# Kernel optimization log

Hardware: AMD Instinct MI355X
Metric: run time of the kernel (lower is better)

## Reference

```python
import jax, jax.numpy as jnp
import numpy as np

D_MODEL = 1024
N_HEADS = 16
D_HEAD = D_MODEL // N_HEADS
B, S = 2, 2048


def setup_inputs() -> dict:
    key = jax.random.key(0)
    ks = jax.random.split(key, 8)
    scale = 1.0 / np.sqrt(D_MODEL)
    return {
        "x": jax.random.normal(ks[0], (B, S, D_MODEL), dtype=jnp.float32),
        "Wq": jax.random.normal(ks[1], (D_MODEL, D_MODEL), dtype=jnp.float32) * scale,
        "bq": jnp.zeros((D_MODEL,), dtype=jnp.float32),
        "Wk": jax.random.normal(ks[2], (D_MODEL, D_MODEL), dtype=jnp.float32) * scale,
        "bk": jnp.zeros((D_MODEL,), dtype=jnp.float32),
        "Wv": jax.random.normal(ks[3], (D_MODEL, D_MODEL), dtype=jnp.float32) * scale,
        "bv": jnp.zeros((D_MODEL,), dtype=jnp.float32),
        "Wo": jax.random.normal(ks[4], (D_MODEL, D_MODEL), dtype=jnp.float32) * scale,
    }


def reference(x, Wq, bq, Wk, bk, Wv, bv, Wo):
    Bsz, Slen, D = x.shape
    # projections -> [B, H, S, Dh]
    def split_heads(t):
        return t.reshape(Bsz, Slen, N_HEADS, D_HEAD).transpose(0, 2, 1, 3)
    q = split_heads(x @ Wq + bq)
    k = split_heads(x @ Wk + bk)
    v = split_heads(x @ Wv + bv)
    scale = jnp.sqrt(jnp.float32(D_HEAD))
    scores = jnp.einsum('bhsd,bhtd->bhst', q, k) / scale  # [B,H,S,S]
    causal_mask = jnp.tril(jnp.ones((Slen, Slen), dtype=jnp.bool_))
    scores = jnp.where(causal_mask, scores, jnp.finfo(scores.dtype).min)
    attn = jax.nn.softmax(scores, axis=-1)
    # deterministic=True path: dropout is identity
    out = jnp.einsum('bhst,bhtd->bhsd', attn, v)
    out = out.transpose(0, 2, 1, 3).reshape(Bsz, Slen, D)
    return out @ Wo
```

## Files before the change

### kernel.cpp

```cpp
#include <hip/hip_runtime.h>
#include <hip/hip_bf16.h>

#define BATCH   2
#define SEQ     2048
#define DMODEL  1024
#define NHEADS  16
#define DHEAD   64
#define MROWS   (BATCH*SEQ)
#define NBH     (BATCH*NHEADS)

typedef float  f32x4  __attribute__((ext_vector_type(4)));
typedef short  s16x4  __attribute__((ext_vector_type(4)));
typedef short  s16x8  __attribute__((ext_vector_type(8)));
typedef __bf16 bf16x8 __attribute__((ext_vector_type(8)));

__device__ __forceinline__ short f2bf(float f) {
  union { float f; unsigned u; } v; v.f = f;
  return (short)((v.u + 0x7fffu + ((v.u >> 16) & 1u)) >> 16);
}
__device__ __forceinline__ float bf2f(short s) {
  union { unsigned u; float f; } v; v.u = ((unsigned)(unsigned short)s) << 16;
  return v.f;
}

__global__ void convert_x(const float* __restrict__ x, short* __restrict__ xb) {
  int i = (blockIdx.x * 256 + threadIdx.x) * 4;
  float4 v = *(const float4*)(x + i);
  s16x4 o = { f2bf(v.x), f2bf(v.y), f2bf(v.z), f2bf(v.w) };
  *(s16x4*)(xb + i) = o;
}

__global__ void transpose_w(const float* __restrict__ Wq, const float* __restrict__ Wk,
                            const float* __restrict__ Wv, const float* __restrict__ Wo,
                            short* __restrict__ WtQKV, short* __restrict__ WtO) {
  __shared__ float t[32][33];
  const float* W; short* Wt;
  int z = blockIdx.z;
  if      (z == 0) { W = Wq; Wt = WtQKV; }
  else if (z == 1) { W = Wk; Wt = WtQKV + (1u << 20); }
  else if (z == 2) { W = Wv; Wt = WtQKV + (2u << 20); }
  else             { W = Wo; Wt = WtO; }
  int n0 = blockIdx.x * 32, k0 = blockIdx.y * 32;
  int tx = threadIdx.x, ty = threadIdx.y;
  #pragma unroll
  for (int i = 0; i < 32; i += 8) t[ty + i][tx] = W[(k0 + ty + i) * DMODEL + n0 + tx];
  __syncthreads();
  #pragma unroll
  for (int i = 0; i < 32; i += 8) Wt[(n0 + ty + i) * DMODEL + k0 + tx] = f2bf(t[tx][ty + i]);
}

template<int MT, int NT, int EPI>
__global__ __launch_bounds__(256) void gemm_bf16(
    const short* __restrict__ A, const short* __restrict__ Bt,
    const float* __restrict__ bq, const float* __restrict__ bk, const float* __restrict__ bv,
    short* __restrict__ qb, short* __restrict__ kb, short* __restrict__ vt,
    float* __restrict__ out)
{
  constexpr int K = DMODEL, BK = 32;
  constexpr int WM = MT / 2, WN = NT / 2;
  constexpr int TM = WM / 16, TN = WN / 16;
  constexpr int CA = MT * BK / 512;
  constexpr int CB = NT * BK / 512;
  constexpr int TP = 136;
  constexpr int SME = (EPI == 0) ? 128 * TP : (MT * BK + NT * BK);
  __shared__ short smem[SME];
  short* la = smem;
  short* lb = smem + MT * BK;
  const int tid = threadIdx.x;
  const int wave = tid >> 6, lane = tid & 63;
  const int quad = lane >> 4, l16 = lane & 15;
  const int wr = wave >> 1, wc = wave & 1;
  const int m0 = blockIdx.y * MT, n0 = blockIdx.x * NT;
  const int arow = lane >> 2, acol = (lane & 3) * 8;

  f32x4 acc[TM][TN] = {};

  for (int k0 = 0; k0 < K; k0 += BK) {
    for (int c = wave; c < CA; c += 4) {
      const short* gp = A + (m0 + c * 16 + arow) * K + k0 + acol;
      __builtin_amdgcn_global_load_lds((__attribute__((address_space(1))) void*)gp,
                                       (__attribute__((address_space(3))) void*)(la + c * 512),
                                       16, 0, 0);
    }
    for (int c = wave; c < CB; c += 4) {
      const short* gp = Bt + (n0 + c * 16 + arow) * K + k0 + acol;
      __builtin_amdgcn_global_load_lds((__attribute__((address_space(1))) void*)gp,
                                       (__attribute__((address_space(3))) void*)(lb + c * 512),
                                       16, 0, 0);
    }
    __syncthreads();
    bf16x8 af[TM], bfr[TN];
    #pragma unroll
    for (int i = 0; i < TM; ++i)
      af[i] = *(const bf16x8*)&la[(wr * WM + i * 16 + l16) * BK + quad * 8];
    #pragma unroll
    for (int j = 0; j < TN; ++j)
      bfr[j] = *(const bf16x8*)&lb[(wc * WN + j * 16 + l16) * BK + quad * 8];
    #pragma unroll
    for (int i = 0; i < TM; ++i)
      #pragma unroll
      for (int j = 0; j < TN; ++j)
        acc[i][j] = __builtin_amdgcn_mfma_f32_16x16x32_bf16(af[i], bfr[j], acc[i][j], 0, 0, 0);
    __syncthreads();
  }

  if constexpr (EPI == 0) {
    const bool isV = (n0 >= 2 * DMODEL);
    const float* bias; int nbase; float scl;
    if (n0 < DMODEL)          { bias = bq; nbase = 0;          scl = 0.125f * 1.44269504089f; }
    else if (n0 < 2 * DMODEL) { bias = bk; nbase = DMODEL;     scl = 1.f; }
    else                      { bias = bv; nbase = 2 * DMODEL; scl = 1.f; }
    #pragma unroll
    for (int j = 0; j < TN; ++j) {
      int coll = wc * WN + j * 16 + l16;
      float bias_v = bias[n0 - nbase + coll];
      #pragma unroll
      for (int i = 0; i < TM; ++i) {
        int rowl = wr * WM + i * 16 + quad * 4;
        #pragma unroll
        for (int r = 0; r < 4; ++r) {
          short v = f2bf((acc[i][j][r] + bias_v) * scl);
          if (isV) smem[coll * TP + rowl + r] = v;
          else     smem[(rowl + r) * TP + coll] = v;
        }
      }
    }
    __syncthreads();
    const int b = m0 >> 11, s0 = m0 & (SEQ - 1);
    const int rseg = tid & 15, rrow = tid >> 4;
    if (!isV) {
      short* dst = (n0 < DMODEL) ? qb : kb;
      #pragma unroll
      for (int it = 0; it < 8; ++it) {
        int row = it * 16 + rrow;
        int colg = (n0 - nbase) + rseg * 8;
        int h = colg >> 6, d = colg & 63;
        s16x8 v = *(const s16x8*)&smem[row * TP + rseg * 8];
        *(s16x8*)(dst + ((b * NHEADS + h) * SEQ + s0 + row) * DHEAD + d) = v;
      }
    } else {
      #pragma unroll
      for (int it = 0; it < 8; ++it) {
        int drow = it * 16 + rrow;
        int colg = (n0 - nbase) + drow;
        int h = colg >> 6, d = colg & 63;
        s16x8 v = *(const s16x8*)&smem[drow * TP + rseg * 8];
        *(s16x8*)(vt + ((b * NHEADS + h) * DHEAD + d) * SEQ + s0 + rseg * 8) = v;
      }
    }
  } else {
    #pragma unroll
    for (int i = 0; i < TM; ++i)
      #pragma unroll
      for (int r = 0; r < 4; ++r) {
        int mrow = m0 + wr * WM + i * 16 + quad * 4 + r;
        #pragma unroll
        for (int j = 0; j < TN; ++j)
          out[mrow * DMODEL + n0 + wc * WN + j * 16 + l16] = acc[i][j][r];
      }
    (void)bq; (void)bk; (void)bv; (void)qb; (void)kb; (void)vt;
  }
}


__global__ __launch_bounds__(256, 2) void attn_k(
    const short* __restrict__ qbp, const short* __restrict__ kbp,
    const short* __restrict__ vtb, short* __restrict__ oP, float* __restrict__ lP)
{
  __shared__ short kls[2][4096];
  __shared__ short vls[2][4096];
  const int tid = threadIdx.x, wave = tid >> 6, lane = tid & 63;
  const int quad = lane >> 4, l16 = lane & 15;
  const int half = blockIdx.x & 1;
  const int bh = (blockIdx.x >> 1) & 31;
  const int qg = blockIdx.x >> 6;
  const int qt = qg * 4 + wave;
  const int ma = qt * 16;
  const int mb = (127 - qt) * 16;
  const int nch = (127 - qg * 4) / 4 + 1;
  const short* Q  = qbp + bh * SEQ * DHEAD;
  const short* Kp = kbp + bh * SEQ * DHEAD;
  const short* Vt = vtb + bh * DHEAD * SEQ;

  bf16x8 qa0 = *(const bf16x8*)&Q[(ma + l16) * DHEAD + quad * 8];
  bf16x8 qa1 = *(const bf16x8*)&Q[(ma + l16) * DHEAD + 32 + quad * 8];
  bf16x8 qb0 = *(const bf16x8*)&Q[(mb + l16) * DHEAD + quad * 8];
  bf16x8 qb1 = *(const bf16x8*)&Q[(mb + l16) * DHEAD + 32 + quad * 8];

  float lA = 0.f, lB = 0.f;
  f32x4 oA[4] = {}, oB[4] = {};

  const int vdl = lane >> 3, vsl = lane & 7;

  auto stage = [&](int buf, int t0) {
    #pragma unroll
    for (int j = 0; j < 2; ++j) {
      int g = j * 4 + wave;
      const short* gp = Kp + (t0 + lane) * DHEAD + g * 8;
      __builtin_amdgcn_global_load_lds((__attribute__((address_space(1))) void*)gp,
                                       (__attribute__((address_space(3))) void*)&kls[buf][g * 512],
                                       16, 0, 0);
    }
    #pragma unroll
    for (int j = 0; j < 2; ++j) {
      int gd = j * 4 + wave;
      const short* gp = Vt + (gd * 8 + vdl) * SEQ + t0 + ((vsl ^ vdl) * 8);
      __builtin_amdgcn_global_load_lds((__attribute__((address_space(1))) void*)gp,
                                       (__attribute__((address_space(3))) void*)&vls[buf][gd * 512],
                                       16, 0, 0);
    }
  };

  auto frag = [&](const bf16x8 kf[4][2], const s16x4 vf[4][4], int t0, int mF,
                  bf16x8 f0, bf16x8 f1, float& lF, f32x4 oF[4]) {
    const int nlive = (mF - t0) / 16 + 1;
    #pragma unroll
    for (int t = 0; t < 4; ++t) {
      if (t < nlive) {
        f32x4 a = {};
        a = __builtin_amdgcn_mfma_f32_16x16x32_bf16(kf[t][0], f0, a, 0, 0, 0);
        a = __builtin_amdgcn_mfma_f32_16x16x32_bf16(kf[t][1], f1, a, 0, 0, 0);
        if (t0 + t * 16 == mF) {
          #pragma unroll
          for (int r = 0; r < 4; ++r)
            if (quad * 4 + r > l16) a[r] = -1e30f;
        }
        f32x4 p;
        #pragma unroll
        for (int r = 0; r < 4; ++r) p[r] = __builtin_amdgcn_exp2f(a[r]);
        lF += (p[0] + p[1]) + (p[2] + p[3]);
        __hip_bfloat162 c01 = __float22bfloat162_rn(float2{p[0], p[1]});
        __hip_bfloat162 c23 = __float22bfloat162_rn(float2{p[2], p[3]});
        union { unsigned u[2]; s16x4 s; } pu;
        pu.u[0] = *(unsigned*)&c01; pu.u[1] = *(unsigned*)&c23;
        #pragma unroll
        for (int dt = 0; dt < 4; ++dt)
          oF[dt] = __builtin_amdgcn_mfma_f32_16x16x16bf16_1k(pu.s, vf[t][dt], oF[dt], 0, 0, 0);
      }
    }
  };

  stage(0, half * 64);
  for (int c = half; c < nch; c += 2) {
    __syncthreads();
    if (c + 2 < nch) stage(((c >> 1) + 1) & 1, (c + 2) * 64);
    const int t0 = c * 64;
    const int buf = (c >> 1) & 1;
    bf16x8 kf[4][2];
    #pragma unroll
    for (int t = 0; t < 4; ++t)
      #pragma unroll
      for (int h = 0; h < 2; ++h)
        kf[t][h] = *(const bf16x8*)&kls[buf][((h * 4 + quad) * 64 + t * 16 + l16) * 8];
    s16x4 vf[4][4];
    #pragma unroll
    for (int t = 0; t < 4; ++t) {
      int gsw = ((t * 2 + (quad >> 1)) ^ (l16 & 7));
      #pragma unroll
      for (int dt = 0; dt < 4; ++dt)
        vf[t][dt] = *(const s16x4*)&vls[buf][((dt * 16 + l16) * 8 + gsw) * 8 + (quad & 1) * 4];
    }
    if (t0 <= mb) frag(kf, vf, t0, mb, qb0, qb1, lB, oB);
    if (t0 <= ma) frag(kf, vf, t0, ma, qa0, qa1, lA, oA);
  }

  lA += __shfl_xor(lA, 16, 64); lA += __shfl_xor(lA, 32, 64);
  lB += __shfl_xor(lB, 16, 64); lB += __shfl_xor(lB, 32, 64);
  float* lD = lP + (half * NBH + bh) * SEQ;
  if (quad == 0) { lD[ma + l16] = lA; lD[mb + l16] = lB; }
  short* oD = oP + ((half * NBH + bh) * SEQ) * DHEAD;
  #pragma unroll
  for (int r = 0; r < 4; ++r) {
    int sA = ma + quad * 4 + r, sB = mb + quad * 4 + r;
    #pragma unroll
    for (int dt = 0; dt < 4; ++dt) {
      oD[sA * DHEAD + dt * 16 + l16] = f2bf(oA[dt][r]);
      oD[sB * DHEAD + dt * 16 + l16] = f2bf(oB[dt][r]);
    }
  }
}

__global__ void attn_merge(const short* __restrict__ oP, const float* __restrict__ lP,
                           short* __restrict__ ob) {
  int idx = blockIdx.x * 256 + threadIdx.x;
  int d8 = idx & 7, s = (idx >> 3) & (SEQ - 1), bh = idx >> 14;
  s16x8 e = *(const s16x8*)&oP[((0   + bh) * SEQ + s) * DHEAD + d8 * 8];
  s16x8 o = *(const s16x8*)&oP[((NBH + bh) * SEQ + s) * DHEAD + d8 * 8];
  float linv = 1.0f / (lP[bh * SEQ + s] + lP[(NBH + bh) * SEQ + s]);
  s16x8 r;
  #pragma unroll
  for (int k = 0; k < 8; ++k) r[k] = f2bf((bf2f(e[k]) + bf2f(o[k])) * linv);
  int b = bh >> 4, h = bh & 15;
  *(s16x8*)&ob[(b * SEQ + s) * DMODEL + h * DHEAD + d8 * 8] = r;
}

extern "C" void kernel_launch(void* const* d_in, const int* in_sizes, int n_in,
                              void* d_out, int out_size, void* d_ws, size_t ws_size,
                              hipStream_t stream) {
  const float* x  = (const float*)d_in[0];
  const float* Wq = (const float*)d_in[1];
  const float* bq = (const float*)d_in[2];
  const float* Wk = (const float*)d_in[3];
  const float* bk = (const float*)d_in[4];
  const float* Wv = (const float*)d_in[5];
  const float* bv = (const float*)d_in[6];
  const float* Wo = (const float*)d_in[7];
  float* out = (float*)d_out;

  char* ws = (char*)d_ws;
  short* xb  = (short*)(ws);
  short* wtq = (short*)(ws + (8u  << 20));
  short* oP  = (short*)(ws);
  short* qb  = (short*)(ws + (16u << 20));
  short* kb  = (short*)(ws + (24u << 20));
  short* vt  = (short*)(ws + (32u << 20));
  short* ob  = (short*)(ws + (40u << 20));
  short* wto = (short*)(ws + (48u << 20));
  float* lP  = (float*)(ws + (50u << 20));

  convert_x<<<MROWS * DMODEL / 1024, 256, 0, stream>>>(x, xb);
  transpose_w<<<dim3(32, 32, 4), dim3(32, 8), 0, stream>>>(Wq, Wk, Wv, Wo, wtq, wto);

  gemm_bf16<128, 128, 0><<<dim3(3 * DMODEL / 128, MROWS / 128), 256, 0, stream>>>(
      xb, wtq, bq, bk, bv, qb, kb, vt, nullptr);

  attn_k<<<NBH * 16 * 2, 256, 0, stream>>>(qb, kb, vt, oP, lP);
  attn_merge<<<NBH * SEQ * 8 / 256, 256, 0, stream>>>(oP, lP, ob);

  gemm_bf16<64, 128, 1><<<dim3(DMODEL / 128, MROWS / 64), 256, 0, stream>>>(
      ob, wto, nullptr, nullptr, nullptr, nullptr, nullptr, nullptr, out);
}
```

Baseline: 198.6 us.

## Process four query tiles per wave in attention to reuse K/V fragments

Each wave of the attention kernel now handles four 16-row query tiles: two adjacent tiles from the front and their mirrored pair from the back, instead of one front/back pair. K and V fragments read from LDS are shared across all four tiles, and the grid is halved. This cuts LDS reads and global K/V staging per unit of work. The cost is more accumulator registers (16 f32x4 plus 8 Q fragments) and half as many blocks, which may reduce occupancy and parallelism on the device.

```diff
diff --git a/kernel.cpp b/kernel.cpp
--- a/kernel.cpp
+++ b/kernel.cpp
@@ -174,21 +174,22 @@
   const int half = blockIdx.x & 1;
   const int bh = (blockIdx.x >> 1) & 31;
   const int qg = blockIdx.x >> 6;
-  const int qt = qg * 4 + wave;
-  const int ma = qt * 16;
-  const int mb = (127 - qt) * 16;
-  const int nch = (127 - qg * 4) / 4 + 1;
+  const int qt1 = qg * 8 + wave * 2;
+  const int mF[4] = { qt1 * 16, (qt1 + 1) * 16, (126 - qt1) * 16, (127 - qt1) * 16 };
+  const int nch = (127 - 8 * qg) / 4 + 1;
   const short* Q  = qbp + bh * SEQ * DHEAD;
   const short* Kp = kbp + bh * SEQ * DHEAD;
   const short* Vt = vtb + bh * DHEAD * SEQ;
 
-  bf16x8 qa0 = *(const bf16x8*)&Q[(ma + l16) * DHEAD + quad * 8];
-  bf16x8 qa1 = *(const bf16x8*)&Q[(ma + l16) * DHEAD + 32 + quad * 8];
-  bf16x8 qb0 = *(const bf16x8*)&Q[(mb + l16) * DHEAD + quad * 8];
-  bf16x8 qb1 = *(const bf16x8*)&Q[(mb + l16) * DHEAD + 32 + quad * 8];
-
-  float lA = 0.f, lB = 0.f;
-  f32x4 oA[4] = {}, oB[4] = {};
+  bf16x8 qf[4][2];
+  #pragma unroll
+  for (int f = 0; f < 4; ++f) {
+    qf[f][0] = *(const bf16x8*)&Q[(mF[f] + l16) * DHEAD + quad * 8];
+    qf[f][1] = *(const bf16x8*)&Q[(mF[f] + l16) * DHEAD + 32 + quad * 8];
+  }
+
+  float lF[4] = {};
+  f32x4 oF[4][4] = {};
 
   const int vdl = lane >> 3, vsl = lane & 7;
 
@@ -211,71 +212,66 @@
     }
   };
 
-  auto frag = [&](const bf16x8 kf[4][2], const s16x4 vf[4][4], int t0, int mF,
-                  bf16x8 f0, bf16x8 f1, float& lF, f32x4 oF[4]) {
-    const int nlive = (mF - t0) / 16 + 1;
-    #pragma unroll
-    for (int t = 0; t < 4; ++t) {
-      if (t < nlive) {
-        f32x4 a = {};
-        a = __builtin_amdgcn_mfma_f32_16x16x32_bf16(kf[t][0], f0, a, 0, 0, 0);
-        a = __builtin_amdgcn_mfma_f32_16x16x32_bf16(kf[t][1], f1, a, 0, 0, 0);
-        if (t0 + t * 16 == mF) {
-          #pragma unroll
-          for (int r = 0; r < 4; ++r)
-            if (quad * 4 + r > l16) a[r] = -1e30f;
-        }
-        f32x4 p;
-        #pragma unroll
-        for (int r = 0; r < 4; ++r) p[r] = __builtin_amdgcn_exp2f(a[r]);
-        lF += (p[0] + p[1]) + (p[2] + p[3]);
-        __hip_bfloat162 c01 = __float22bfloat162_rn(float2{p[0], p[1]});
-        __hip_bfloat162 c23 = __float22bfloat162_rn(float2{p[2], p[3]});
-        union { unsigned u[2]; s16x4 s; } pu;
-        pu.u[0] = *(unsigned*)&c01; pu.u[1] = *(unsigned*)&c23;
-        #pragma unroll
-        for (int dt = 0; dt < 4; ++dt)
-          oF[dt] = __builtin_amdgcn_mfma_f32_16x16x16bf16_1k(pu.s, vf[t][dt], oF[dt], 0, 0, 0);
-      }
-    }
-  };
-
   stage(0, half * 64);
   for (int c = half; c < nch; c += 2) {
     __syncthreads();
     if (c + 2 < nch) stage(((c >> 1) + 1) & 1, (c + 2) * 64);
     const int t0 = c * 64;
     const int buf = (c >> 1) & 1;
-    bf16x8 kf[4][2];
-    #pragma unroll
-    for (int t = 0; t < 4; ++t)
-      #pragma unroll
-      for (int h = 0; h < 2; ++h)
-        kf[t][h] = *(const bf16x8*)&kls[buf][((h * 4 + quad) * 64 + t * 16 + l16) * 8];
-    s16x4 vf[4][4];
     #pragma unroll
     for (int t = 0; t < 4; ++t) {
-      int gsw = ((t * 2 + (quad >> 1)) ^ (l16 & 7));
+      const int tb = t0 + t * 16;
+      if (tb <= mF[3]) {
+        bf16x8 kf0 = *(const bf16x8*)&kls[buf][((0 + quad) * 64 + t * 16 + l16) * 8];
+        bf16x8 kf1 = *(const bf16x8*)&kls[buf][((4 + quad) * 64 + t * 16 + l16) * 8];
+        s16x4 vf[4];
+        {
+          int gsw = ((t * 2 + (quad >> 1)) ^ (l16 & 7));
+          #pragma unroll
+          for (int dt = 0; dt < 4; ++dt)
+            vf[dt] = *(const s16x4*)&vls[buf][((dt * 16 + l16) * 8 + gsw) * 8 + (quad & 1) * 4];
+        }
+        #pragma unroll
+        for (int f = 0; f < 4; ++f) {
+          if (tb <= mF[f]) {
+            f32x4 a = {};
+            a = __builtin_amdgcn_mfma_f32_16x16x32_bf16(kf0, qf[f][0], a, 0, 0, 0);
+            a = __builtin_amdgcn_mfma_f32_16x16x32_bf16(kf1, qf[f][1], a, 0, 0, 0);
+            if (tb == mF[f]) {
+              #pragma unroll
+              for (int r = 0; r < 4; ++r)
+                if (quad * 4 + r > l16) a[r] = -1e30f;
+            }
+            f32x4 p;
+            #pragma unroll
+            for (int r = 0; r < 4; ++r) p[r] = __builtin_amdgcn_exp2f(a[r]);
+            lF[f] += (p[0] + p[1]) + (p[2] + p[3]);
+            __hip_bfloat162 c01 = __float22bfloat162_rn(float2{p[0], p[1]});
+            __hip_bfloat162 c23 = __float22bfloat162_rn(float2{p[2], p[3]});
+            union { unsigned u[2]; s16x4 s; } pu;
+            pu.u[0] = *(unsigned*)&c01; pu.u[1] = *(unsigned*)&c23;
+            #pragma unroll
+            for (int dt = 0; dt < 4; ++dt)
+              oF[f][dt] = __builtin_amdgcn_mfma_f32_16x16x16bf16_1k(pu.s, vf[dt], oF[f][dt], 0, 0, 0);
+          }
+        }
+      }
+    }
+  }
+
+  float* lD = lP + (half * NBH + bh) * SEQ;
+  short* oD = oP + ((half * NBH + bh) * SEQ) * DHEAD;
+  #pragma unroll
+  for (int f = 0; f < 4; ++f) {
+    float l = lF[f];
+    l += __shfl_xor(l, 16, 64); l += __shfl_xor(l, 32, 64);
+    if (quad == 0) lD[mF[f] + l16] = l;
+    #pragma unroll
+    for (int r = 0; r < 4; ++r) {
+      int s = mF[f] + quad * 4 + r;
       #pragma unroll
       for (int dt = 0; dt < 4; ++dt)
-        vf[t][dt] = *(const s16x4*)&vls[buf][((dt * 16 + l16) * 8 + gsw) * 8 + (quad & 1) * 4];
-    }
-    if (t0 <= mb) frag(kf, vf, t0, mb, qb0, qb1, lB, oB);
-    if (t0 <= ma) frag(kf, vf, t0, ma, qa0, qa1, lA, oA);
-  }
-
-  lA += __shfl_xor(lA, 16, 64); lA += __shfl_xor(lA, 32, 64);
-  lB += __shfl_xor(lB, 16, 64); lB += __shfl_xor(lB, 32, 64);
-  float* lD = lP + (half * NBH + bh) * SEQ;
-  if (quad == 0) { lD[ma + l16] = lA; lD[mb + l16] = lB; }
-  short* oD = oP + ((half * NBH + bh) * SEQ) * DHEAD;
-  #pragma unroll
-  for (int r = 0; r < 4; ++r) {
-    int sA = ma + quad * 4 + r, sB = mb + quad * 4 + r;
-    #pragma unroll
-    for (int dt = 0; dt < 4; ++dt) {
-      oD[sA * DHEAD + dt * 16 + l16] = f2bf(oA[dt][r]);
-      oD[sB * DHEAD + dt * 16 + l16] = f2bf(oB[dt][r]);
+        oD[s * DHEAD + dt * 16 + l16] = f2bf(oF[f][dt][r]);
     }
   }
 }
@@ -324,7 +320,7 @@
   gemm_bf16<128, 128, 0><<<dim3(3 * DMODEL / 128, MROWS / 128), 256, 0, stream>>>(
       xb, wtq, bq, bk, bv, qb, kb, vt, nullptr);
 
-  attn_k<<<NBH * 16 * 2, 256, 0, stream>>>(qb, kb, vt, oP, lP);
+  attn_k<<<NBH * 8 * 2, 256, 0, stream>>>(qb, kb, vt, oP, lP);
   attn_merge<<<NBH * SEQ * 8 / 256, 256, 0, stream>>>(oP, lP, ob);
 
   gemm_bf16<64, 128, 1><<<dim3(DMODEL / 128, MROWS / 64), 256, 0, stream>>>(
```

After: 192.9 us. -2.8%, faster.
